# Optimization experiments

Measured on AMD Instinct MI355X. Metric: run time of the kernel, lower is better.

## Reference

```python
import jax, jax.numpy as jnp
import numpy as np

N = 100000; E = 3200000; F_IN = 128; H1 = 32; H2 = 64; G = 256; ACT = 64

def _leaky(x):
    return jnp.where(x > 0, x, 0.1 * x)

def _gcn(x, W, b, src, dst, n):
    # PyG GCNConv: h = x @ W; add self-loops; symmetric deg^{-1/2} normalization;
    # scatter-add messages from src to dst; add bias.
    h = x @ W
    loops = jnp.arange(n, dtype=src.dtype)
    s = jnp.concatenate([src, loops])
    d = jnp.concatenate([dst, loops])
    deg = jax.ops.segment_sum(jnp.ones(s.shape[0], h.dtype), d, num_segments=n)
    dinv = jax.lax.rsqrt(jnp.maximum(deg, 1.0))  # deg >= 1 thanks to self-loops
    norm = dinv[s] * dinv[d]                      # [E+N]
    agg = jax.ops.segment_sum(h[s] * norm[:, None], d, num_segments=n)
    return agg + b

def setup_inputs():
    key = jax.random.key(0)
    k = jax.random.split(key, 8)
    x = jax.random.normal(k[0], (N, F_IN), jnp.float32)
    edge_index = jax.random.randint(k[1], (2, E), 0, N, dtype=jnp.int32)
    # sorted segment ids, 256 graphs of ~N/G nodes each (no empty segments)
    batch = ((jnp.arange(N) * G) // N).astype(jnp.int32)
    s = 0.05
    W1 = jax.random.normal(k[2], (F_IN, H1), jnp.float32) * s; b1 = jnp.zeros((H1,), jnp.float32)
    W2 = jax.random.normal(k[3], (H1, H2), jnp.float32) * s;   b2 = jnp.zeros((H2,), jnp.float32)
    l1W = jax.random.normal(k[4], (H2, 128), jnp.float32) * s; l1b = jnp.zeros((128,), jnp.float32)
    l2W = jax.random.normal(k[5], (128, 64), jnp.float32) * s; l2b = jnp.zeros((64,), jnp.float32)
    l3W = jax.random.normal(k[6], (64, ACT), jnp.float32) * s; l3b = jnp.zeros((ACT,), jnp.float32)
    return dict(x=x, edge_index=edge_index, batch=batch, W1=W1, b1=b1, W2=W2, b2=b2,
                l1W=l1W, l1b=l1b, l2W=l2W, l2b=l2b, l3W=l3W, l3b=l3b)

def reference(x, edge_index, batch, W1, b1, W2, b2, l1W, l1b, l2W, l2b, l3W, l3b):
    src, dst = edge_index[0], edge_index[1]
    h = _leaky(_gcn(x, W1, b1, src, dst, N))      # [N, 32]
    h = _gcn(h, W2, b2, src, dst, N)              # [N, 64]
    g = jax.ops.segment_max(h, batch, num_segments=G)  # global_max_pool -> [G, 64]
    z = _leaky(g @ l1W + l1b)
    z = _leaky(z @ l2W + l2b)
    return z @ l3W + l3b                          # [G, n_actions]
```

## Files before the change

kernel.cpp:

```cpp
#include <hip/hip_runtime.h>
#include <math.h>

#define N_NODES 100000
#define N_EDGES 3200000
#define F_INPUT 128
#define H1DIM 32
#define H2DIM 64
#define NGRAPH 256
#define NACT 64
#define EPB 16384
#define NBLK_A ((N_EDGES + EPB - 1) / EPB)
#define NBUCK ((N_NODES + 255) / 256)

typedef _Float16 half4 __attribute__((ext_vector_type(4)));
typedef _Float16 half8 __attribute__((ext_vector_type(8)));

__global__ __launch_bounds__(1024) void binhist_kernel(const int* __restrict__ dst,
                                                       int* __restrict__ countsA, int e)
{
    __shared__ int hist[NBUCK];
    for (int i = threadIdx.x; i < NBUCK; i += 1024) hist[i] = 0;
    __syncthreads();
    int beg = blockIdx.x * EPB, end = min(beg + EPB, e);
    for (int i = beg + threadIdx.x; i < end; i += 1024)
        atomicAdd(&hist[dst[i] >> 8], 1);
    __syncthreads();
    for (int i = threadIdx.x; i < NBUCK; i += 1024)
        countsA[blockIdx.x * NBUCK + i] = hist[i];
}

__global__ __launch_bounds__(64) void scanAp_kernel(int* __restrict__ countsA,
                                                    int* __restrict__ bucketTot)
{
    int b = blockIdx.x;
    int lane = threadIdx.x;
    int carry = 0;
    for (int r = 0; r < (NBLK_A + 63) / 64; ++r) {
        int blk = r * 64 + lane;
        int v = (blk < NBLK_A) ? countsA[blk * NBUCK + b] : 0;
        int own = v;
        for (int d = 1; d < 64; d <<= 1) {
            int t = __shfl_up(v, d);
            if (lane >= d) v += t;
        }
        if (blk < NBLK_A) countsA[blk * NBUCK + b] = v - own + carry;
        carry += __shfl(v, 63);
    }
    if (lane == 0) bucketTot[b] = carry;
}

__global__ __launch_bounds__(512) void scanB_kernel(const int* __restrict__ bucketTot,
                                                    int* __restrict__ bucketBase,
                                                    int* __restrict__ rowptr,
                                                    float* __restrict__ g)
{
    __shared__ int sums[512];
    int b = threadIdx.x;
    int own = (b < NBUCK) ? bucketTot[b] : 0;
    sums[b] = own;
    __syncthreads();
    for (int off = 1; off < 512; off <<= 1) {
        int v = (b >= off) ? sums[b - off] : 0;
        __syncthreads();
        sums[b] += v;
        __syncthreads();
    }
    if (b < NBUCK) bucketBase[b] = sums[b] - own;
    if (b == 0) { bucketBase[NBUCK] = N_EDGES; rowptr[N_NODES] = N_EDGES; }
    for (int i = b; i < NGRAPH * H2DIM; i += 512) g[i] = -INFINITY;
}

__global__ __launch_bounds__(1024) void binplace_kernel(const int* __restrict__ src,
                                                        const int* __restrict__ dst,
                                                        const int* __restrict__ countsA,
                                                        const int* __restrict__ bucketBase,
                                                        int* __restrict__ binned, int e)
{
    __shared__ int cur[NBUCK];
    for (int i = threadIdx.x; i < NBUCK; i += 1024)
        cur[i] = countsA[blockIdx.x * NBUCK + i] + bucketBase[i];
    __syncthreads();
    int beg = blockIdx.x * EPB, end = min(beg + EPB, e);
    for (int i = beg + threadIdx.x; i < end; i += 1024) {
        int d = dst[i], s = src[i];
        int pos = atomicAdd(&cur[d >> 8], 1);
        binned[pos] = ((d & 255) << 17) | s;
    }
}

__global__ __launch_bounds__(256) void csr_kernel(const int* __restrict__ binned,
                                                  const int* __restrict__ bucketBase,
                                                  int* __restrict__ srcsorted,
                                                  int* __restrict__ rowptr,
                                                  float* __restrict__ dinv, int n)
{
    __shared__ int hist[256];
    __shared__ int sc[256];
    int b = blockIdx.x, t = threadIdx.x;
    hist[t] = 0;
    __syncthreads();
    int eBeg = bucketBase[b], eEnd = bucketBase[b + 1];
    for (int i = eBeg + t; i < eEnd; i += 256)
        atomicAdd(&hist[binned[i] >> 17], 1);
    __syncthreads();
    int own = hist[t];
    sc[t] = own;
    __syncthreads();
    for (int off = 1; off < 256; off <<= 1) {
        int v = (t >= off) ? sc[t - off] : 0;
        __syncthreads();
        sc[t] += v;
        __syncthreads();
    }
    int excl = sc[t] - own;
    int node = b * 256 + t;
    if (node < n) {
        rowptr[node] = eBeg + excl;
        dinv[node] = 1.0f / sqrtf((float)(own + 1));
    }
    hist[t] = eBeg + excl;
    __syncthreads();
    for (int i = eBeg + t; i < eEnd; i += 256) {
        int v = binned[i];
        int pos = atomicAdd(&hist[v >> 17], 1);
        srcsorted[pos] = v & 0x1FFFF;
    }
}

__global__ __launch_bounds__(256) void gemm_scale_f16_kernel(
    const float* __restrict__ x, const float* __restrict__ W,
    const float* __restrict__ dinv, _Float16* __restrict__ out, int n)
{
    constexpr int KDIM = F_INPUT, NOUT = H1DIM;
    constexpr int KH = 64;
    constexpr int ROWS = 64;
    constexpr int XS = KH + 4;
    constexpr int CG = NOUT / 8;
    __shared__ float xs[ROWS * XS];
    __shared__ float Ws[KH * NOUT];
    int t = threadIdx.x;
    int row0 = blockIdx.x * ROWS;
    int tcg = t % CG;
    int trow = t / CG;

    float acc[8];
#pragma unroll
    for (int j = 0; j < 8; ++j) acc[j] = 0.f;

    for (int h = 0; h < 2; ++h) {
        if (h) __syncthreads();
        for (int i = t; i < KH * NOUT; i += 256) Ws[i] = W[h * KH * NOUT + i];
        for (int i = t; i < ROWS * (KH / 4); i += 256) {
            int r = i / (KH / 4);
            int kk = i % (KH / 4);
            float4 v = make_float4(0.f, 0.f, 0.f, 0.f);
            if (row0 + r < n)
                v = ((const float4*)x)[(size_t)(row0 + r) * (KDIM / 4) + h * (KH / 4) + kk];
            *(float4*)&xs[r * XS + kk * 4] = v;
        }
        __syncthreads();

#pragma unroll
        for (int k = 0; k < KH; k += 4) {
            float4 xv = *(float4*)&xs[trow * XS + k];
#pragma unroll
            for (int kk = 0; kk < 4; ++kk) {
                float4 w0 = *(float4*)&Ws[(k + kk) * NOUT + tcg * 8];
                float4 w1 = *(float4*)&Ws[(k + kk) * NOUT + tcg * 8 + 4];
                float xk = ((float*)&xv)[kk];
                acc[0] += xk * w0.x; acc[1] += xk * w0.y;
                acc[2] += xk * w0.z; acc[3] += xk * w0.w;
                acc[4] += xk * w1.x; acc[5] += xk * w1.y;
                acc[6] += xk * w1.z; acc[7] += xk * w1.w;
            }
        }
    }

    int row = row0 + trow;
    if (row < n) {
        float dv = dinv[row];
        half8 o;
#pragma unroll
        for (int j = 0; j < 8; ++j) o[j] = (_Float16)(acc[j] * dv);
        *(half8*)&out[(size_t)row * NOUT + tcg * 8] = o;
    }
}

template<int MODE, typename OutV>
__global__ __launch_bounds__(256) void agg16_kernel(
    const _Float16* __restrict__ tmp, const int* __restrict__ rowptr,
    const int* __restrict__ srcs, const float* __restrict__ dinv,
    const float* __restrict__ bias, OutV* __restrict__ out, int n)
{
    constexpr int FG = H1DIM / 4;
    int tid = blockIdx.x * blockDim.x + threadIdx.x;
    int node = tid / FG;
    int fg = tid % FG;
    if (node >= n) return;
    int beg = rowptr[node], end = rowptr[node + 1];
    const half4* t4 = (const half4*)tmp;
    half4 sv = t4[(size_t)node * FG + fg];
    float ax = (float)sv.x, ay = (float)sv.y, az = (float)sv.z, aw = (float)sv.w;
    int j = beg;
    for (; j + 8 <= end; j += 8) {
        int s0 = srcs[j],     s1 = srcs[j + 1], s2 = srcs[j + 2], s3 = srcs[j + 3];
        int s4 = srcs[j + 4], s5 = srcs[j + 5], s6 = srcs[j + 6], s7 = srcs[j + 7];
        half4 v0 = t4[(size_t)s0 * FG + fg];
        half4 v1 = t4[(size_t)s1 * FG + fg];
        half4 v2 = t4[(size_t)s2 * FG + fg];
        half4 v3 = t4[(size_t)s3 * FG + fg];
        half4 v4 = t4[(size_t)s4 * FG + fg];
        half4 v5 = t4[(size_t)s5 * FG + fg];
        half4 v6 = t4[(size_t)s6 * FG + fg];
        half4 v7 = t4[(size_t)s7 * FG + fg];
        ax += (float)v0.x + (float)v1.x + (float)v2.x + (float)v3.x
            + (float)v4.x + (float)v5.x + (float)v6.x + (float)v7.x;
        ay += (float)v0.y + (float)v1.y + (float)v2.y + (float)v3.y
            + (float)v4.y + (float)v5.y + (float)v6.y + (float)v7.y;
        az += (float)v0.z + (float)v1.z + (float)v2.z + (float)v3.z
            + (float)v4.z + (float)v5.z + (float)v6.z + (float)v7.z;
        aw += (float)v0.w + (float)v1.w + (float)v2.w + (float)v3.w
            + (float)v4.w + (float)v5.w + (float)v6.w + (float)v7.w;
    }
    for (; j < end; ++j) {
        half4 v = t4[(size_t)srcs[j] * FG + fg];
        ax += (float)v.x; ay += (float)v.y; az += (float)v.z; aw += (float)v.w;
    }
    float dv = dinv[node];
    if (MODE == 0) {
        float4 bb = ((const float4*)bias)[fg];
        float rx = ax * dv + bb.x, ry = ay * dv + bb.y;
        float rz = az * dv + bb.z, rw = aw * dv + bb.w;
        rx = (rx > 0.f) ? rx : 0.1f * rx;
        ry = (ry > 0.f) ? ry : 0.1f * ry;
        rz = (rz > 0.f) ? rz : 0.1f * rz;
        rw = (rw > 0.f) ? rw : 0.1f * rw;
        half4 o;
        o.x = (_Float16)(rx * dv); o.y = (_Float16)(ry * dv);
        o.z = (_Float16)(rz * dv); o.w = (_Float16)(rw * dv);
        ((half4*)out)[(size_t)node * FG + fg] = o;
    } else {
        float4 o;
        o.x = ax * dv; o.y = ay * dv; o.z = az * dv; o.w = aw * dv;
        ((float4*)out)[(size_t)node * FG + fg] = o;
    }
}

__device__ inline void atomicMaxFloat(float* addr, float val)
{
    if (val >= 0.f) atomicMax((int*)addr, __float_as_int(val));
    else            atomicMin((unsigned int*)addr, __float_as_uint(val));
}

__global__ __launch_bounds__(256) void gemmsegmax_kernel(
    const float* __restrict__ a, const float* __restrict__ W2,
    const float* __restrict__ b2, float* __restrict__ g, int n)
{
    __shared__ float Ws[H1DIM * H2DIM];
    __shared__ float rows[64 * H1DIM];
    __shared__ float redA[256], redB[256];
    int t = threadIdx.x;
    int base = blockIdx.x * 64;
    int lim = min(base + 64, n);
    for (int i = t; i < H1DIM * H2DIM; i += 256) Ws[i] = W2[i];
    {
        const float4* a4 = (const float4*)a;
        int nf4 = (lim - base) * (H1DIM / 4);
        for (int i = t; i < nf4; i += 256)
            ((float4*)rows)[i] = a4[(size_t)base * (H1DIM / 4) + i];
    }
    __syncthreads();
    int sub = t >> 6, f = t & 63;
    float wreg[H1DIM];
#pragma unroll
    for (int k = 0; k < H1DIM; ++k) wreg[k] = Ws[k * H2DIM + f];
    float bf = b2[f];
    int gidA = (int)(((long long)base * NGRAPH) / n);
    float mA = -INFINITY, mB = -INFINITY;
    for (int i = base + sub; i < lim; i += 4) {
        float acc = bf;
        int lr = i - base;
#pragma unroll
        for (int k = 0; k < H1DIM; k += 4) {
            float4 rv = *(float4*)&rows[lr * H1DIM + k];
            acc += rv.x * wreg[k] + rv.y * wreg[k + 1]
                 + rv.z * wreg[k + 2] + rv.w * wreg[k + 3];
        }
        int gid = (int)(((long long)i * NGRAPH) / n);
        if (gid == gidA) mA = fmaxf(mA, acc);
        else             mB = fmaxf(mB, acc);
    }
    redA[t] = mA; redB[t] = mB;
    __syncthreads();
    if (t < 64) {
        float v = fmaxf(fmaxf(redA[t], redA[t + 64]), fmaxf(redA[t + 128], redA[t + 192]));
        if (v > -INFINITY) atomicMaxFloat(&g[gidA * H2DIM + t], v);
    } else if (t < 128) {
        int f2 = t - 64;
        float v = fmaxf(fmaxf(redB[f2], redB[f2 + 64]), fmaxf(redB[f2 + 128], redB[f2 + 192]));
        int gidB = gidA + 1;
        if (gidB < NGRAPH && v > -INFINITY) atomicMaxFloat(&g[gidB * H2DIM + f2], v);
    }
}

__global__ __launch_bounds__(128) void mlp_kernel(
    const float* __restrict__ g,
    const float* __restrict__ l1W, const float* __restrict__ l1b,
    const float* __restrict__ l2W, const float* __restrict__ l2b,
    const float* __restrict__ l3W, const float* __restrict__ l3b,
    float* __restrict__ out)
{
    __shared__ float gin[64], z1[128], z2[64];
    int b = blockIdx.x, t = threadIdx.x;
    if (t < 64) gin[t] = g[b * 64 + t];
    __syncthreads();
    {
        float a = l1b[t];
        for (int k = 0; k < 64; ++k) a += gin[k] * l1W[k * 128 + t];
        z1[t] = (a > 0.f) ? a : 0.1f * a;
    }
    __syncthreads();
    if (t < 64) {
        float a = l2b[t];
        for (int k = 0; k < 128; ++k) a += z1[k] * l2W[k * 64 + t];
        z2[t] = (a > 0.f) ? a : 0.1f * a;
    }
    __syncthreads();
    if (t < 64) {
        float a = l3b[t];
        for (int k = 0; k < 64; ++k) a += z2[k] * l3W[k * 64 + t];
        out[b * 64 + t] = a;
    }
}

extern "C" void kernel_launch(void* const* d_in, const int* in_sizes, int n_in,
                              void* d_out, int out_size, void* d_ws, size_t ws_size,
                              hipStream_t stream) {
    const float* x   = (const float*)d_in[0];
    const int*   ei  = (const int*)d_in[1];
    const int*   src = ei;
    const int*   dst = ei + N_EDGES;
    const float* W1  = (const float*)d_in[3];
    const float* b1  = (const float*)d_in[4];
    const float* W2  = (const float*)d_in[5];
    const float* b2  = (const float*)d_in[6];
    const float* l1W = (const float*)d_in[7];
    const float* l1b = (const float*)d_in[8];
    const float* l2W = (const float*)d_in[9];
    const float* l2b = (const float*)d_in[10];
    const float* l3W = (const float*)d_in[11];
    const float* l3b = (const float*)d_in[12];
    float* outp = (float*)d_out;

    char* w = (char*)d_ws;
    size_t off = 0;
    auto alloc = [&](size_t bytes) { char* p = w + off; off += (bytes + 255) & ~(size_t)255; return p; };
    int*   countsA    = (int*)  alloc((size_t)NBLK_A * NBUCK * sizeof(int));
    int*   bucketTot  = (int*)  alloc(NBUCK * sizeof(int));
    int*   bucketBase = (int*)  alloc((NBUCK + 1) * sizeof(int));
    int*   rowptr     = (int*)  alloc((N_NODES + 1) * sizeof(int));
    float* dinv       = (float*)alloc(N_NODES * sizeof(float));
    int*   srcsorted  = (int*)  alloc(N_EDGES * sizeof(int));
    float* bufA       = (float*)alloc((size_t)N_NODES * 64 * sizeof(float));
    float* bufB       = (float*)alloc((size_t)N_NODES * 32 * sizeof(float));
    float* gbuf       = (float*)alloc(NGRAPH * H2DIM * sizeof(float));

    _Float16* tmp1 = (_Float16*)bufA;
    _Float16* s1   = (_Float16*)bufB;
    float*    abuf = bufA;
    int* binned = (int*)(bufA + (size_t)N_NODES * 32);

    binhist_kernel<<<NBLK_A, 1024, 0, stream>>>(dst, countsA, N_EDGES);
    scanAp_kernel<<<NBUCK, 64, 0, stream>>>(countsA, bucketTot);
    scanB_kernel<<<1, 512, 0, stream>>>(bucketTot, bucketBase, rowptr, gbuf);
    binplace_kernel<<<NBLK_A, 1024, 0, stream>>>(src, dst, countsA, bucketBase, binned, N_EDGES);
    csr_kernel<<<NBUCK, 256, 0, stream>>>(binned, bucketBase, srcsorted, rowptr, dinv, N_NODES);

    gemm_scale_f16_kernel<<<(N_NODES + 63) / 64, 256, 0, stream>>>(x, W1, dinv, tmp1, N_NODES);
    agg16_kernel<0, half4><<<((size_t)N_NODES * (H1DIM/4) + 255) / 256, 256, 0, stream>>>(
        tmp1, rowptr, srcsorted, dinv, b1, (half4*)s1, N_NODES);
    agg16_kernel<1, float4><<<((size_t)N_NODES * (H1DIM/4) + 255) / 256, 256, 0, stream>>>(
        s1, rowptr, srcsorted, dinv, b1 , (float4*)abuf, N_NODES);

    gemmsegmax_kernel<<<(N_NODES + 63) / 64, 256, 0, stream>>>(abuf, W2, b2, gbuf, N_NODES);
    mlp_kernel<<<NGRAPH, 128, 0, stream>>>(gbuf, l1W, l1b, l2W, l2b, l3W, l3b, outp);
}
```

Measured before the change: 297.6 us.

## Fuse second aggregation into segmax GEMM, merge scan kernels, widen gathers to half8

Folds the single-block bucket scan into the per-bucket scan kernel with a last-block-done counter, and moves the -inf init of the pooled buffer into the CSR kernel. The second 32-wide aggregation is fused into the GEMM+segment-max kernel, so the float32 intermediate is never written to or re-read from global memory. Gathers now use 16-byte half8 loads with 4 threads per node instead of half4 with 8. This removes two launches and one large intermediate round trip. In exchange it relies on a device-wide atomic completion counter, and the fused kernel's aggregation phase may have lower occupancy and less load-level parallelism.

```diff
diff --git a/kernel.cpp b/kernel.cpp
--- a/kernel.cpp
+++ b/kernel.cpp
@@ -16,8 +16,10 @@
 typedef _Float16 half8 __attribute__((ext_vector_type(8)));
 
 __global__ __launch_bounds__(1024) void binhist_kernel(const int* __restrict__ dst,
-                                                       int* __restrict__ countsA, int e)
-{
+                                                       int* __restrict__ countsA,
+                                                       int* __restrict__ done, int e)
+{
+    if (blockIdx.x == 0 && threadIdx.x == 0) *done = 0;
     __shared__ int hist[NBUCK];
     for (int i = threadIdx.x; i < NBUCK; i += 1024) hist[i] = 0;
     __syncthreads();
@@ -29,8 +31,11 @@
         countsA[blockIdx.x * NBUCK + i] = hist[i];
 }
 
-__global__ __launch_bounds__(64) void scanAp_kernel(int* __restrict__ countsA,
-                                                    int* __restrict__ bucketTot)
+__global__ __launch_bounds__(64) void scanApB_kernel(int* __restrict__ countsA,
+                                                     int* __restrict__ bucketTot,
+                                                     int* __restrict__ bucketBase,
+                                                     int* __restrict__ rowptr,
+                                                     int* __restrict__ done)
 {
     int b = blockIdx.x;
     int lane = threadIdx.x;
@@ -47,27 +52,26 @@
         carry += __shfl(v, 63);
     }
     if (lane == 0) bucketTot[b] = carry;
-}
-
-__global__ __launch_bounds__(512) void scanB_kernel(const int* __restrict__ bucketTot,
-                                                    int* __restrict__ bucketBase,
-                                                    int* __restrict__ rowptr,
-                                                    float* __restrict__ g)
-{
-    __shared__ int sums[512];
-    int b = threadIdx.x;
-    int own = (b < NBUCK) ? bucketTot[b] : 0;
-    sums[b] = own;
-    __syncthreads();
-    for (int off = 1; off < 512; off <<= 1) {
-        int v = (b >= off) ? sums[b - off] : 0;
-        __syncthreads();
-        sums[b] += v;
-        __syncthreads();
-    }
-    if (b < NBUCK) bucketBase[b] = sums[b] - own;
-    if (b == 0) { bucketBase[NBUCK] = N_EDGES; rowptr[N_NODES] = N_EDGES; }
-    for (int i = b; i < NGRAPH * H2DIM; i += 512) g[i] = -INFINITY;
+    __threadfence();
+    __shared__ int isLast;
+    if (lane == 0) isLast = (atomicAdd(done, 1) == NBUCK - 1);
+    __syncthreads();
+    if (isLast) {
+        __threadfence();
+        int carry2 = 0;
+        for (int r = 0; r < (NBUCK + 63) / 64; ++r) {
+            int i = r * 64 + lane;
+            int v = (i < NBUCK) ? atomicAdd(&bucketTot[i], 0) : 0;
+            int own = v;
+            for (int d = 1; d < 64; d <<= 1) {
+                int t = __shfl_up(v, d);
+                if (lane >= d) v += t;
+            }
+            if (i < NBUCK) bucketBase[i] = carry2 + v - own;
+            carry2 += __shfl(v, 63);
+        }
+        if (lane == 0) { bucketBase[NBUCK] = N_EDGES; rowptr[N_NODES] = N_EDGES; }
+    }
 }
 
 __global__ __launch_bounds__(1024) void binplace_kernel(const int* __restrict__ src,
@@ -92,11 +96,13 @@
                                                   const int* __restrict__ bucketBase,
                                                   int* __restrict__ srcsorted,
                                                   int* __restrict__ rowptr,
-                                                  float* __restrict__ dinv, int n)
-{
+                                                  float* __restrict__ dinv,
+                                                  float* __restrict__ g, int n)
+{
+    int b = blockIdx.x, t = threadIdx.x;
+    if (b < (NGRAPH * H2DIM) / 256) g[b * 256 + t] = -INFINITY;
     __shared__ int hist[256];
     __shared__ int sc[256];
-    int b = blockIdx.x, t = threadIdx.x;
     hist[t] = 0;
     __syncthreads();
     int eBeg = bucketBase[b], eEnd = bucketBase[b + 1];
@@ -186,64 +192,49 @@
     }
 }
 
-template<int MODE, typename OutV>
-__global__ __launch_bounds__(256) void agg16_kernel(
+__global__ __launch_bounds__(256) void agg1_kernel(
     const _Float16* __restrict__ tmp, const int* __restrict__ rowptr,
     const int* __restrict__ srcs, const float* __restrict__ dinv,
-    const float* __restrict__ bias, OutV* __restrict__ out, int n)
-{
-    constexpr int FG = H1DIM / 4;
+    const float* __restrict__ bias, _Float16* __restrict__ out, int n)
+{
     int tid = blockIdx.x * blockDim.x + threadIdx.x;
-    int node = tid / FG;
-    int fg = tid % FG;
+    int node = tid >> 2;
+    int fq = tid & 3;
     if (node >= n) return;
     int beg = rowptr[node], end = rowptr[node + 1];
-    const half4* t4 = (const half4*)tmp;
-    half4 sv = t4[(size_t)node * FG + fg];
-    float ax = (float)sv.x, ay = (float)sv.y, az = (float)sv.z, aw = (float)sv.w;
+    const half8* t8 = (const half8*)tmp;
+    half8 sv = t8[(size_t)node * 4 + fq];
+    float acc[8];
+#pragma unroll
+    for (int q = 0; q < 8; ++q) acc[q] = (float)sv[q];
     int j = beg;
-    for (; j + 8 <= end; j += 8) {
-        int s0 = srcs[j],     s1 = srcs[j + 1], s2 = srcs[j + 2], s3 = srcs[j + 3];
-        int s4 = srcs[j + 4], s5 = srcs[j + 5], s6 = srcs[j + 6], s7 = srcs[j + 7];
-        half4 v0 = t4[(size_t)s0 * FG + fg];
-        half4 v1 = t4[(size_t)s1 * FG + fg];
-        half4 v2 = t4[(size_t)s2 * FG + fg];
-        half4 v3 = t4[(size_t)s3 * FG + fg];
-        half4 v4 = t4[(size_t)s4 * FG + fg];
-        half4 v5 = t4[(size_t)s5 * FG + fg];
-        half4 v6 = t4[(size_t)s6 * FG + fg];
-        half4 v7 = t4[(size_t)s7 * FG + fg];
-        ax += (float)v0.x + (float)v1.x + (float)v2.x + (float)v3.x
-            + (float)v4.x + (float)v5.x + (float)v6.x + (float)v7.x;
-        ay += (float)v0.y + (float)v1.y + (float)v2.y + (float)v3.y
-            + (float)v4.y + (float)v5.y + (float)v6.y + (float)v7.y;
-        az += (float)v0.z + (float)v1.z + (float)v2.z + (float)v3.z
-            + (float)v4.z + (float)v5.z + (float)v6.z + (float)v7.z;
-        aw += (float)v0.w + (float)v1.w + (float)v2.w + (float)v3.w
-            + (float)v4.w + (float)v5.w + (float)v6.w + (float)v7.w;
+    for (; j + 4 <= end; j += 4) {
+        int s0 = srcs[j], s1 = srcs[j + 1], s2 = srcs[j + 2], s3 = srcs[j + 3];
+        half8 v0 = t8[(size_t)s0 * 4 + fq];
+        half8 v1 = t8[(size_t)s1 * 4 + fq];
+        half8 v2 = t8[(size_t)s2 * 4 + fq];
+        half8 v3 = t8[(size_t)s3 * 4 + fq];
+#pragma unroll
+        for (int q = 0; q < 8; ++q)
+            acc[q] += (float)v0[q] + (float)v1[q] + (float)v2[q] + (float)v3[q];
     }
     for (; j < end; ++j) {
-        half4 v = t4[(size_t)srcs[j] * FG + fg];
-        ax += (float)v.x; ay += (float)v.y; az += (float)v.z; aw += (float)v.w;
+        half8 v = t8[(size_t)srcs[j] * 4 + fq];
+#pragma unroll
+        for (int q = 0; q < 8; ++q) acc[q] += (float)v[q];
     }
     float dv = dinv[node];
-    if (MODE == 0) {
-        float4 bb = ((const float4*)bias)[fg];
-        float rx = ax * dv + bb.x, ry = ay * dv + bb.y;
-        float rz = az * dv + bb.z, rw = aw * dv + bb.w;
-        rx = (rx > 0.f) ? rx : 0.1f * rx;
-        ry = (ry > 0.f) ? ry : 0.1f * ry;
-        rz = (rz > 0.f) ? rz : 0.1f * rz;
-        rw = (rw > 0.f) ? rw : 0.1f * rw;
-        half4 o;
-        o.x = (_Float16)(rx * dv); o.y = (_Float16)(ry * dv);
-        o.z = (_Float16)(rz * dv); o.w = (_Float16)(rw * dv);
-        ((half4*)out)[(size_t)node * FG + fg] = o;
-    } else {
-        float4 o;
-        o.x = ax * dv; o.y = ay * dv; o.z = az * dv; o.w = aw * dv;
-        ((float4*)out)[(size_t)node * FG + fg] = o;
-    }
+    float bb[8];
+    *(float4*)&bb[0] = ((const float4*)bias)[fq * 2];
+    *(float4*)&bb[4] = ((const float4*)bias)[fq * 2 + 1];
+    half8 o;
+#pragma unroll
+    for (int q = 0; q < 8; ++q) {
+        float r = acc[q] * dv + bb[q];
+        r = (r > 0.f) ? r : 0.1f * r;
+        o[q] = (_Float16)(r * dv);
+    }
+    ((half8*)out)[(size_t)node * 4 + fq] = o;
 }
 
 __device__ inline void atomicMaxFloat(float* addr, float val)
@@ -252,9 +243,11 @@
     else            atomicMin((unsigned int*)addr, __float_as_uint(val));
 }
 
-__global__ __launch_bounds__(256) void gemmsegmax_kernel(
-    const float* __restrict__ a, const float* __restrict__ W2,
-    const float* __restrict__ b2, float* __restrict__ g, int n)
+__global__ __launch_bounds__(256) void aggsegmax_kernel(
+    const _Float16* __restrict__ s1, const int* __restrict__ rowptr,
+    const int* __restrict__ srcs, const float* __restrict__ dinv,
+    const float* __restrict__ W2, const float* __restrict__ b2,
+    float* __restrict__ g, int n)
 {
     __shared__ float Ws[H1DIM * H2DIM];
     __shared__ float rows[64 * H1DIM];
@@ -263,13 +256,41 @@
     int base = blockIdx.x * 64;
     int lim = min(base + 64, n);
     for (int i = t; i < H1DIM * H2DIM; i += 256) Ws[i] = W2[i];
+
     {
-        const float4* a4 = (const float4*)a;
-        int nf4 = (lim - base) * (H1DIM / 4);
-        for (int i = t; i < nf4; i += 256)
-            ((float4*)rows)[i] = a4[(size_t)base * (H1DIM / 4) + i];
-    }
-    __syncthreads();
+        int ln = t >> 2;
+        int fq = t & 3;
+        int node = base + ln;
+        if (node < lim) {
+            int beg = rowptr[node], end = rowptr[node + 1];
+            const half8* t8 = (const half8*)s1;
+            half8 sv = t8[(size_t)node * 4 + fq];
+            float acc[8];
+#pragma unroll
+            for (int q = 0; q < 8; ++q) acc[q] = (float)sv[q];
+            int j = beg;
+            for (; j + 4 <= end; j += 4) {
+                int s0 = srcs[j], s1i = srcs[j + 1], s2 = srcs[j + 2], s3 = srcs[j + 3];
+                half8 v0 = t8[(size_t)s0 * 4 + fq];
+                half8 v1 = t8[(size_t)s1i * 4 + fq];
+                half8 v2 = t8[(size_t)s2 * 4 + fq];
+                half8 v3 = t8[(size_t)s3 * 4 + fq];
+#pragma unroll
+                for (int q = 0; q < 8; ++q)
+                    acc[q] += (float)v0[q] + (float)v1[q] + (float)v2[q] + (float)v3[q];
+            }
+            for (; j < end; ++j) {
+                half8 v = t8[(size_t)srcs[j] * 4 + fq];
+#pragma unroll
+                for (int q = 0; q < 8; ++q) acc[q] += (float)v[q];
+            }
+            float dv = dinv[node];
+#pragma unroll
+            for (int q = 0; q < 8; ++q) rows[ln * H1DIM + fq * 8 + q] = acc[q] * dv;
+        }
+    }
+    __syncthreads();
+
     int sub = t >> 6, f = t & 63;
     float wreg[H1DIM];
 #pragma unroll
@@ -358,6 +379,7 @@
     int*   countsA    = (int*)  alloc((size_t)NBLK_A * NBUCK * sizeof(int));
     int*   bucketTot  = (int*)  alloc(NBUCK * sizeof(int));
     int*   bucketBase = (int*)  alloc((NBUCK + 1) * sizeof(int));
+    int*   doneCnt    = (int*)  alloc(sizeof(int));
     int*   rowptr     = (int*)  alloc((N_NODES + 1) * sizeof(int));
     float* dinv       = (float*)alloc(N_NODES * sizeof(float));
     int*   srcsorted  = (int*)  alloc(N_EDGES * sizeof(int));
@@ -367,21 +389,17 @@
 
     _Float16* tmp1 = (_Float16*)bufA;
     _Float16* s1   = (_Float16*)bufB;
-    float*    abuf = bufA;
     int* binned = (int*)(bufA + (size_t)N_NODES * 32);
 
-    binhist_kernel<<<NBLK_A, 1024, 0, stream>>>(dst, countsA, N_EDGES);
-    scanAp_kernel<<<NBUCK, 64, 0, stream>>>(countsA, bucketTot);
-    scanB_kernel<<<1, 512, 0, stream>>>(bucketTot, bucketBase, rowptr, gbuf);
+    binhist_kernel<<<NBLK_A, 1024, 0, stream>>>(dst, countsA, doneCnt, N_EDGES);
+    scanApB_kernel<<<NBUCK, 64, 0, stream>>>(countsA, bucketTot, bucketBase, rowptr, doneCnt);
     binplace_kernel<<<NBLK_A, 1024, 0, stream>>>(src, dst, countsA, bucketBase, binned, N_EDGES);
-    csr_kernel<<<NBUCK, 256, 0, stream>>>(binned, bucketBase, srcsorted, rowptr, dinv, N_NODES);
+    csr_kernel<<<NBUCK, 256, 0, stream>>>(binned, bucketBase, srcsorted, rowptr, dinv, gbuf, N_NODES);
 
     gemm_scale_f16_kernel<<<(N_NODES + 63) / 64, 256, 0, stream>>>(x, W1, dinv, tmp1, N_NODES);
-    agg16_kernel<0, half4><<<((size_t)N_NODES * (H1DIM/4) + 255) / 256, 256, 0, stream>>>(
-        tmp1, rowptr, srcsorted, dinv, b1, (half4*)s1, N_NODES);
-    agg16_kernel<1, float4><<<((size_t)N_NODES * (H1DIM/4) + 255) / 256, 256, 0, stream>>>(
-        s1, rowptr, srcsorted, dinv, b1 , (float4*)abuf, N_NODES);
-
-    gemmsegmax_kernel<<<(N_NODES + 63) / 64, 256, 0, stream>>>(abuf, W2, b2, gbuf, N_NODES);
+    agg1_kernel<<<((size_t)N_NODES * 4 + 255) / 256, 256, 0, stream>>>(
+        tmp1, rowptr, srcsorted, dinv, b1, s1, N_NODES);
+    aggsegmax_kernel<<<(N_NODES + 63) / 64, 256, 0, stream>>>(
+        s1, rowptr, srcsorted, dinv, W2, b2, gbuf, N_NODES);
     mlp_kernel<<<NGRAPH, 128, 0, stream>>>(gbuf, l1W, l1b, l2W, l2b, l3W, l3b, outp);
 }
```

Result: slower. 314.9 us (+5.8%).
